# Performance work log

Hardware: AMD Instinct MI355X
Metric: run time of the kernel (lower is better)

The kernel has to match this reference:

```python
import jax, jax.numpy as jnp
import numpy as np
from jax import lax

B, MID, OUT, H, W = 16, 128, 512, 112, 112
EPS = 1e-5


def _conv(x, w, stride=1, pad=0, dil=1, groups=1):
    return lax.conv_general_dilated(
        x, w, window_strides=(stride, stride),
        padding=[(pad, pad), (pad, pad)], rhs_dilation=(dil, dil),
        feature_group_count=groups,
        dimension_numbers=('NCHW', 'OIHW', 'NCHW'))


def setup_inputs() -> dict:
    key = jax.random.key(0)
    ks = jax.random.split(key, 12)
    s = 0.05
    return {
        'x': jax.random.normal(ks[0], (B, 2 * MID, H, W), jnp.float32),
        # kernel_gen: Linear(mid, mid*9, bias=False) weight [mid*9, mid]
        'W_kg': jax.random.normal(ks[1], (MID * 9, MID), jnp.float32) * s,
        # global stream: depthwise 3x3 dil=2, then 1x1 conv, BN
        'gdw_w': jax.random.normal(ks[2], (MID, 1, 3, 3), jnp.float32) * s,
        'gdw_b': jax.random.normal(ks[3], (MID,), jnp.float32) * s,
        'gpw_w': jax.random.normal(ks[4], (MID, MID, 1, 1), jnp.float32) * s,
        'gpw_b': jax.random.normal(ks[5], (MID,), jnp.float32) * s,
        'bn1_g': jnp.ones((MID,), jnp.float32),
        'bn1_b': jnp.zeros((MID,), jnp.float32),
        'bn1_m': jax.random.normal(ks[6], (MID,), jnp.float32) * s,
        'bn1_v': jax.random.uniform(ks[7], (MID,), jnp.float32, 0.5, 1.5),
        # downsample: Conv2d(2*mid, out, 3, stride=2, pad=1), BN
        'ds_w': jax.random.normal(ks[8], (OUT, 2 * MID, 3, 3), jnp.float32) * s,
        'ds_b': jax.random.normal(ks[9], (OUT,), jnp.float32) * s,
        'bn2_g': jnp.ones((OUT,), jnp.float32),
        'bn2_b': jnp.zeros((OUT,), jnp.float32),
        'bn2_m': jax.random.normal(ks[10], (OUT,), jnp.float32) * s,
        'bn2_v': jax.random.uniform(ks[11], (OUT,), jnp.float32, 0.5, 1.5),
    }


def _bn(x, g, b, m, v):  # eval-mode BatchNorm2d
    inv = g / jnp.sqrt(v + EPS)
    return x * inv[None, :, None, None] + (b - m * inv)[None, :, None, None]


def reference(x, W_kg, gdw_w, gdw_b, gpw_w, gpw_b,
              bn1_g, bn1_b, bn1_m, bn1_v,
              ds_w, ds_b, bn2_g, bn2_b, bn2_m, bn2_v):
    local_in, global_in = jnp.split(x, 2, axis=1)  # [B,MID,H,W] each
    b, c, h, w = local_in.shape

    # local branch: pool -> linear+relu kernel-gen -> per-sample depthwise 3x3
    pooled = jnp.mean(local_in, axis=(2, 3))                  # [b,c]
    kernels = jax.nn.relu(pooled @ W_kg.T)                    # [b, c*9]
    kernels = kernels.reshape(b * c, 1, 3, 3)
    local_out = _conv(local_in.reshape(1, b * c, h, w), kernels,
                      pad=1, groups=b * c).reshape(b, c, h, w)

    # global branch: depthwise dil-2 conv -> 1x1 conv -> BN -> ReLU
    g = _conv(global_in, gdw_w, pad=2, dil=2, groups=c) + gdw_b[None, :, None, None]
    g = _conv(g, gpw_w) + gpw_b[None, :, None, None]
    g = jax.nn.relu(_bn(g, bn1_g, bn1_b, bn1_m, bn1_v))

    combined = jnp.concatenate([local_out, g], axis=1)        # [b,2c,h,w]
    out = _conv(combined, ds_w, stride=2, pad=1) + ds_b[None, :, None, None]
    out = jax.nn.relu(_bn(out, bn2_g, bn2_b, bn2_m, bn2_v))   # [b,OUT,h/2,w/2]
    return out
```

## Files before the change

### kernel.cpp

```cpp
#include <hip/hip_runtime.h>


#define DEVI static __device__ __forceinline__

using bf16x8 = __attribute__((ext_vector_type(8))) short;
using f32x4  = __attribute__((ext_vector_type(4))) float;
typedef unsigned short ushort_t;

constexpr int Bn = 16, MID = 128, CHN = 256, Hh = 112, Wn = 112;
constexpr int OHn = 56, OWn = 56, OCn = 512;
constexpr int HW  = Hh * Wn;
constexpr float EPSf = 1e-5f;

constexpr size_t C_I = 56 * 64;
constexpr size_t C_P = 4 * C_I;
constexpr size_t C_H = 2 * C_P;
constexpr size_t C_B = (size_t)Hh * C_H;

DEVI ushort_t f2b(float f) {
    unsigned u = __float_as_uint(f);
    return (ushort_t)((u + 0x7FFFu + ((u >> 16) & 1u)) >> 16);
}
DEVI float b2f(ushort_t s) { return __uint_as_float(((unsigned)s) << 16); }
DEVI int pack2(float a, float b) {
    return (int)f2b(a) | ((int)f2b(b) << 16);
}

DEVI void gl_lds16(const void* g, void* l) {
    __builtin_amdgcn_global_load_lds(
        (const __attribute__((address_space(1))) unsigned int*)g,
        (__attribute__((address_space(3))) unsigned int*)l, 16, 0, 0);
}

__global__ __launch_bounds__(256) void k_prep(
        const float* __restrict__ gpw_w, const float* __restrict__ gpw_b,
        const float* __restrict__ bn1g, const float* __restrict__ bn1b,
        const float* __restrict__ bn1m, const float* __restrict__ bn1v,
        const float* __restrict__ dsb,
        const float* __restrict__ bn2g, const float* __restrict__ bn2b,
        const float* __restrict__ bn2m, const float* __restrict__ bn2v,
        ushort_t* __restrict__ gpwbf,
        float* __restrict__ a1, float* __restrict__ b1,
        float* __restrict__ a2, float* __restrict__ b2,
        float* __restrict__ pooled) {
    int i = blockIdx.x * 256 + threadIdx.x;
    if (i < MID * MID) gpwbf[i] = f2b(gpw_w[i]);
    if (i < Bn * MID) pooled[i] = 0.f;
    if (i < OCn) {
        float inv = bn2g[i] / sqrtf(bn2v[i] + EPSf);
        a2[i] = inv;
        b2[i] = bn2b[i] + (dsb[i] - bn2m[i]) * inv;
    }
    if (i < MID) {
        float inv = bn1g[i] / sqrtf(bn1v[i] + EPSf);
        a1[i] = inv;
        b1[i] = bn1b[i] + (gpw_b[i] - bn1m[i]) * inv;
    }
}

__global__ __launch_bounds__(256) void k_wds(const float* __restrict__ dsw,
                                             ushort_t* __restrict__ wds2) {
    int d = blockIdx.x * 256 + threadIdx.x;
    int j = d & 63, oc = (d >> 6) & 511, kb = d >> 15;
    int khw = kb >> 2, icc = kb & 3;
    int ph = j >> 3, c = ph ^ (oc & 7);
    int ic = icc * 64 + c * 8 + (j & 7);
    wds2[d] = f2b(dsw[((size_t)oc * CHN + ic) * 9 + khw]);
}

__global__ __launch_bounds__(256) void k_kgen(const float* __restrict__ pooled,
                                              const float* __restrict__ wkg,
                                              float* __restrict__ kgen) {
    int idx = blockIdx.x * 256 + threadIdx.x;
    int b = idx / 1152, j = idx % 1152;
    int c = j & 127, tp = j >> 7;
    const float* pr = pooled + b * MID;
    const float* wr = wkg + (size_t)(c * 9 + tp) * MID;
    float s = 0.f;
#pragma unroll 8
    for (int i = 0; i < MID; i++) s += pr[i] * wr[i];
    kgen[idx] = fmaxf(s * (1.f / HW), 0.f);
}

__global__ __launch_bounds__(256) void k_xt(const float* __restrict__ x,
                                            ushort_t* __restrict__ xT,
                                            float* __restrict__ pooled) {
    __shared__ ushort_t tile[Wn * 264];
    int t = threadIdx.x;
    int bh = blockIdx.x;
    int b = bh / Hh, h = bh % Hh;
    const float* xp = x + ((size_t)b * CHN * Hh + h) * Wn;
    for (int idx = t; idx < CHN * 28; idx += 256) {
        int ch = idx / 28, q = idx % 28;
        float4 v = *(const float4*)(xp + (size_t)ch * HW + q * 4);
        int w = q * 4;
        tile[w * 264 + ch]       = f2b(v.x);
        tile[(w + 1) * 264 + ch] = f2b(v.y);
        tile[(w + 2) * 264 + ch] = f2b(v.z);
        tile[(w + 3) * 264 + ch] = f2b(v.w);
    }
    __syncthreads();
    int4* dst = (int4*)(xT + (size_t)bh * Wn * CHN);
    for (int q = t; q < Wn * CHN / 8; q += 256) {
        int w = q >> 5, c0 = (q & 31) << 3;
        dst[q] = *(const int4*)(tile + w * 264 + c0);
    }
    if (t < MID) {
        float s = 0.f;
        for (int w = 0; w < Wn; w++) s += b2f(tile[w * 264 + t]);
        atomicAdd(&pooled[b * MID + t], s);
    }
}

template <int DIL>
DEVI void dw_accum_row(const ushort_t* __restrict__ rp,
                       const float* __restrict__ wtab, int tb,
                       int c0, int wbase, float (&acc)[7][8]) {
    constexpr int NC = 7 + 2 * DIL;
    float wk[3][8];
#pragma unroll
    for (int dw = 0; dw < 3; dw++) {
        float4 lo = *(const float4*)&wtab[(tb + dw) * 128 + c0];
        float4 hi = *(const float4*)&wtab[(tb + dw) * 128 + c0 + 4];
        wk[dw][0] = lo.x; wk[dw][1] = lo.y; wk[dw][2] = lo.z; wk[dw][3] = lo.w;
        wk[dw][4] = hi.x; wk[dw][5] = hi.y; wk[dw][6] = hi.z; wk[dw][7] = hi.w;
    }
    int4 C[NC];
#pragma unroll
    for (int j = 0; j < NC; j++) {
        int w1 = wbase - DIL + j;
        int4 v = make_int4(0, 0, 0, 0);
        if ((unsigned)w1 < (unsigned)Wn)
            v = *(const int4*)(rp + (size_t)w1 * CHN);
        C[j] = v;
    }
#pragma unroll
    for (int j = 0; j < NC; j++) {
        float f[8];
        {
            unsigned u;
            u = (unsigned)C[j].x;
            f[0] = __uint_as_float(u << 16); f[1] = __uint_as_float(u & 0xffff0000u);
            u = (unsigned)C[j].y;
            f[2] = __uint_as_float(u << 16); f[3] = __uint_as_float(u & 0xffff0000u);
            u = (unsigned)C[j].z;
            f[4] = __uint_as_float(u << 16); f[5] = __uint_as_float(u & 0xffff0000u);
            u = (unsigned)C[j].w;
            f[6] = __uint_as_float(u << 16); f[7] = __uint_as_float(u & 0xffff0000u);
        }
#pragma unroll
        for (int dw = 0; dw < 3; dw++) {
            int i = j - dw * DIL;
            if (i >= 0 && i <= 6) {
#pragma unroll
                for (int k = 0; k < 8; k++) acc[i][k] += wk[dw][k] * f[k];
            }
        }
    }
}

__global__ __launch_bounds__(256, 3) void k_dwl(
        const ushort_t* __restrict__ xT, const float* __restrict__ kgen,
        ushort_t* __restrict__ comb) {
    __shared__ float wtab[1152];
    int t = threadIdx.x;
    int h = blockIdx.x, b = blockIdx.y;
    {
        const float4* src = (const float4*)(kgen + (size_t)b * 1152);
        float4* dstw = (float4*)wtab;
        dstw[t] = src[t];
        if (t < 32) dstw[256 + t] = src[256 + t];
    }
    __syncthreads();
    int cg = t & 15, wl = t >> 4, c0 = cg << 3, wbase = 7 * wl;
    const ushort_t* xb = xT + (size_t)b * HW * CHN + c0;
    float acc[7][8] = {};
#pragma unroll
    for (int dh = -1; dh <= 1; dh++) {
        int h1 = h + dh;
        if ((unsigned)h1 >= (unsigned)Hh) continue;
        dw_accum_row<1>(xb + (size_t)h1 * Wn * CHN, wtab, (dh + 1) * 3,
                        c0, wbase, acc);
    }
    int icc = c0 >> 6, cch = (c0 & 63) >> 3;
#pragma unroll
    for (int i = 0; i < 7; i++) {
        int w = wbase + i;
        int4 O;
        O.x = pack2(acc[i][0], acc[i][1]);
        O.y = pack2(acc[i][2], acc[i][3]);
        O.z = pack2(acc[i][4], acc[i][5]);
        O.w = pack2(acc[i][6], acc[i][7]);
        int w2 = w >> 1, p = w & 1, ph = cch ^ (w2 & 7);
        *(int4*)(comb + (size_t)b * C_B + (size_t)h * C_H + p * C_P
                 + icc * C_I + w2 * 64 + ph * 8) = O;
    }
}

__global__ __launch_bounds__(256, 3) void k_dwg(
        const ushort_t* __restrict__ xT,
        const float* __restrict__ gdw_w, const float* __restrict__ gdw_b,
        const ushort_t* __restrict__ gpwbf,
        const float* __restrict__ a1, const float* __restrict__ b1,
        ushort_t* __restrict__ comb) {
    __shared__ float wtab[1152];
    __shared__ ushort_t pbuf[112 * 136];
    int t = threadIdx.x;
    int h = blockIdx.x, b = blockIdx.y;
    for (int e4 = t; e4 < 288; e4 += 256) {
        float4 v = *(const float4*)(gdw_w + (size_t)e4 * 4);
        int e = e4 * 4;
        wtab[(e % 9) * 128 + e / 9]             = v.x;
        wtab[((e + 1) % 9) * 128 + (e + 1) / 9] = v.y;
        wtab[((e + 2) % 9) * 128 + (e + 2) / 9] = v.z;
        wtab[((e + 3) % 9) * 128 + (e + 3) / 9] = v.w;
    }
    __syncthreads();
    int cg = t & 15, wl = t >> 4, c0 = cg << 3, wbase = 7 * wl;
    const ushort_t* xb = xT + (size_t)b * HW * CHN + MID + c0;
    float acc[7][8];
    {
        float4 b0 = *(const float4*)(gdw_b + c0);
        float4 b4 = *(const float4*)(gdw_b + c0 + 4);
#pragma unroll
        for (int i = 0; i < 7; i++) {
            acc[i][0] = b0.x; acc[i][1] = b0.y; acc[i][2] = b0.z; acc[i][3] = b0.w;
            acc[i][4] = b4.x; acc[i][5] = b4.y; acc[i][6] = b4.z; acc[i][7] = b4.w;
        }
    }
#pragma unroll
    for (int dh = -1; dh <= 1; dh++) {
        int h1 = h + 2 * dh;
        if ((unsigned)h1 >= (unsigned)Hh) continue;
        dw_accum_row<2>(xb + (size_t)h1 * Wn * CHN, wtab, (dh + 1) * 3,
                        c0, wbase, acc);
    }
#pragma unroll
    for (int i = 0; i < 7; i++) {
        int w = wbase + i;
        int4 O;
        O.x = pack2(acc[i][0], acc[i][1]);
        O.y = pack2(acc[i][2], acc[i][3]);
        O.z = pack2(acc[i][4], acc[i][5]);
        O.w = pack2(acc[i][6], acc[i][7]);
        int ph = cg ^ (w & 15);
        *(int4*)(pbuf + (size_t)w * 128 + ph * 8) = O;
    }
    __syncthreads();
    int lane = t & 63, wave = t >> 6;
    int mrow = lane & 15, quad = lane >> 4;
    const short* gw = (const short*)gpwbf;
    f32x4 acc2[7][2] = {};
#pragma unroll
    for (int ks = 0; ks < 4; ks++) {
        bf16x8 bfr[2];
#pragma unroll
        for (int n = 0; n < 2; n++)
            bfr[n] = *(const bf16x8*)(gw + (size_t)(wave * 32 + n * 16 + mrow) * MID
                                         + ks * 32 + quad * 8);
#pragma unroll
        for (int m = 0; m < 7; m++) {
            int ph = (ks * 4 + quad) ^ mrow;
            bf16x8 af = *(const bf16x8*)(pbuf + (size_t)(m * 16 + mrow) * 128 + ph * 8);
#pragma unroll
            for (int n = 0; n < 2; n++)
                acc2[m][n] = __builtin_amdgcn_mfma_f32_16x16x32_bf16(
                    af, bfr[n], acc2[m][n], 0, 0, 0);
        }
    }
    __syncthreads();
#pragma unroll
    for (int m = 0; m < 7; m++)
#pragma unroll
        for (int n = 0; n < 2; n++) {
            int oc2 = wave * 32 + n * 16 + mrow;
            float al = a1[oc2], be = b1[oc2];
#pragma unroll
            for (int r = 0; r < 4; r++) {
                int px = m * 16 + quad * 4 + r;
                pbuf[px * 136 + oc2] = f2b(fmaxf(acc2[m][n][r] * al + be, 0.f));
            }
        }
    __syncthreads();
    for (int ws = 0; ws < 7; ws++) {
        int w = ws * 16 + wl;
        int4 v = *(const int4*)(pbuf + (size_t)w * 136 + c0);
        int w2 = w >> 1, p = w & 1;
        int gch = MID + c0;
        int icc = gch >> 6, cch = (gch & 63) >> 3, ph = cch ^ (w2 & 7);
        *(int4*)(comb + (size_t)b * C_B + (size_t)h * C_H + p * C_P
                 + icc * C_I + w2 * 64 + ph * 8) = v;
    }
}

__global__ __launch_bounds__(256) void k_ds(
        const ushort_t* __restrict__ comb, const ushort_t* __restrict__ wds2,
        const float* __restrict__ a2, const float* __restrict__ b2,
        float* __restrict__ out) {
    __shared__ ushort_t lA[128 * 64];
    __shared__ ushort_t lB[128 * 64];
    int t = threadIdx.x, lane = t & 63, wave = t >> 6;
    int g = blockIdx.x;
    int xcd = g & 7, s = g >> 3;
    int octile = s & 3, pl = s >> 2;
    int pair = xcd * 56 + pl;
    int bb = pair / 28, ohp = pair % 28;
    int oh0 = ohp * 2, oc0 = octile * 128;
    int mrow = lane & 15, quad = lane >> 4;
    int wm = wave & 1, wn = wave >> 1;
    int ak = mrow & 7;

    f32x4 acc[4][4] = {};
    for (int kt = 0; kt < 36; kt++) {
        int khw = kt >> 2, icc = kt & 3;
        int kh = khw / 3, kw = khw - kh * 3;
        int p = (kw == 1) ? 0 : 1;
        bool zh0 = (oh0 == 0) && (kh == 0);
        int ldsShift = (kw == 0) ? 128 : 0;
        __syncthreads();
        if (zh0) {
            int4 z = {0, 0, 0, 0};
            *(int4*)(lB + t * 8) = z;
            *(int4*)(lB + 2048 + t * 8) = z;
        }
        if (kw == 0 && t < 16) {
            int4 z = {0, 0, 0, 0};
            *(int4*)(lB + (t >> 3) * 4096 + (t & 7) * 8) = z;
        }
        const char* asrc = (const char*)wds2
            + ((size_t)kt * 32768 + (size_t)oc0 * 64) * 2 + lane * 16;
#pragma unroll
        for (int i = 0; i < 4; i++) {
            int j = wave * 4 + i;
            gl_lds16(asrc + j * 1024, (char*)lA + j * 1024);
        }
        for (int j = wave; j < 14; j += 4) {
            int osub = (j >= 7) ? 1 : 0, jj = j - osub * 7;
            if (zh0 && osub == 0) continue;
            int r = 2 * oh0 + 2 * osub + kh - 1;
            const char* bsrc = (const char*)comb
                + ((size_t)bb * C_B + (size_t)r * C_H + (size_t)p * C_P
                   + (size_t)icc * C_I) * 2 + jj * 1024 + lane * 16;
            gl_lds16(bsrc, (char*)lB + osub * 8192 + ldsShift + jj * 1024);
        }
        __syncthreads();
        int bk = (mrow + ((kw == 0) ? 7 : 0)) & 7;
#pragma unroll
        for (int ks = 0; ks < 2; ks++) {
            bf16x8 af[4], bf[4];
#pragma unroll
            for (int m = 0; m < 4; m++) {
                int row = wm * 64 + m * 16 + mrow;
                int ph = (ks * 4 + quad) ^ ak;
                af[m] = *(const bf16x8*)(lA + row * 64 + ph * 8);
            }
#pragma unroll
            for (int n = 0; n < 4; n++) {
                int nr = wn * 64 + n * 16 + mrow;
                int ph = (ks * 4 + quad) ^ bk;
                bf[n] = *(const bf16x8*)(lB + nr * 64 + ph * 8);
            }
#pragma unroll
            for (int m = 0; m < 4; m++)
#pragma unroll
                for (int n = 0; n < 4; n++)
                    acc[m][n] = __builtin_amdgcn_mfma_f32_16x16x32_bf16(
                        af[m], bf[n], acc[m][n], 0, 0, 0);
        }
    }
#pragma unroll
    for (int m = 0; m < 4; m++) {
#pragma unroll
        for (int r4 = 0; r4 < 4; r4++) {
            int oc = oc0 + wm * 64 + m * 16 + quad * 4 + r4;
            float al = a2[oc], be = b2[oc];
#pragma unroll
            for (int n = 0; n < 4; n++) {
                int nr = wn * 64 + n * 16 + mrow;
                int osub = nr >> 6, ow = nr & 63;
                if (ow < OWn) {
                    float v = fmaxf(acc[m][n][r4] * al + be, 0.f);
                    out[((size_t)(bb * OCn + oc) * OHn + (oh0 + osub)) * OWn + ow] = v;
                }
            }
        }
    }
}

extern "C" void kernel_launch(void* const* d_in, const int* in_sizes, int n_in,
                              void* d_out, int out_size, void* d_ws, size_t ws_size,
                              hipStream_t stream) {
    const float* x     = (const float*)d_in[0];
    const float* wkg   = (const float*)d_in[1];
    const float* gdw_w = (const float*)d_in[2];
    const float* gdw_b = (const float*)d_in[3];
    const float* gpw_w = (const float*)d_in[4];
    const float* gpw_b = (const float*)d_in[5];
    const float* bn1g  = (const float*)d_in[6];
    const float* bn1b  = (const float*)d_in[7];
    const float* bn1m  = (const float*)d_in[8];
    const float* bn1v  = (const float*)d_in[9];
    const float* dsw   = (const float*)d_in[10];
    const float* dsb   = (const float*)d_in[11];
    const float* bn2g  = (const float*)d_in[12];
    const float* bn2b  = (const float*)d_in[13];
    const float* bn2m  = (const float*)d_in[14];
    const float* bn2v  = (const float*)d_in[15];

    char* ws = (char*)d_ws;
    float*    pooled = (float*)(ws + 0);
    float*    kgen   = (float*)(ws + 8192);
    float*    a1     = (float*)(ws + 81920);
    float*    b1     = (float*)(ws + 82432);
    float*    a2     = (float*)(ws + 82944);
    float*    b2     = (float*)(ws + 84992);
    ushort_t* gpwbf  = (ushort_t*)(ws + 87040);
    ushort_t* wds2   = (ushort_t*)(ws + 119808);
    ushort_t* comb   = (ushort_t*)(ws + 2479104);
    ushort_t* xT  = (ushort_t*)d_out;
    float*    out = (float*)d_out;

    k_prep<<<64, 256, 0, stream>>>(gpw_w, gpw_b, bn1g, bn1b, bn1m, bn1v,
                                   dsb, bn2g, bn2b, bn2m, bn2v,
                                   gpwbf, a1, b1, a2, b2, pooled);
    k_wds <<<4608, 256, 0, stream>>>(dsw, wds2);
    k_xt  <<<1792, 256, 0, stream>>>(x, xT, pooled);
    k_kgen<<<72, 256, 0, stream>>>(pooled, wkg, kgen);
    k_dwg <<<dim3(Hh, Bn), 256, 0, stream>>>(xT, gdw_w, gdw_b, gpwbf,
                                             a1, b1, comb);
    k_dwl <<<dim3(Hh, Bn), 256, 0, stream>>>(xT, kgen, comb);
    k_ds  <<<1792, 256, 0, stream>>>(comb, wds2, a2, b2, out);
}
```

Before: 339.4 us.

## Split global branch into shared depthwise kernel and separate pointwise MFMA kernel

Merges the local and global depthwise convolutions into one kernel launched over twice the batch dimension, with a branch selecting kernel weights and dilation. The global pointwise 1x1 conv plus BN/ReLU moves into a new kernel that reloads the depthwise result from the comb buffer via direct global-to-LDS copies and writes it back in place. This is meant to free the depthwise stage from the large pbuf LDS footprint and MFMA epilogue, improving occupancy, but it adds an extra global round trip of the global-branch intermediate and one more launch.

```diff
diff --git a/kernel.cpp b/kernel.cpp
--- a/kernel.cpp
+++ b/kernel.cpp
@@ -159,30 +159,63 @@
     }
 }
 
-__global__ __launch_bounds__(256, 3) void k_dwl(
+__global__ __launch_bounds__(256, 3) void k_dw(
         const ushort_t* __restrict__ xT, const float* __restrict__ kgen,
+        const float* __restrict__ gdw_w, const float* __restrict__ gdw_b,
         ushort_t* __restrict__ comb) {
     __shared__ float wtab[1152];
     int t = threadIdx.x;
-    int h = blockIdx.x, b = blockIdx.y;
-    {
+    int h = blockIdx.x, by = blockIdx.y;
+    int b = by >> 1, br = by & 1;
+    if (br == 0) {
         const float4* src = (const float4*)(kgen + (size_t)b * 1152);
         float4* dstw = (float4*)wtab;
         dstw[t] = src[t];
         if (t < 32) dstw[256 + t] = src[256 + t];
+    } else {
+        for (int e4 = t; e4 < 288; e4 += 256) {
+            float4 v = *(const float4*)(gdw_w + (size_t)e4 * 4);
+            int e = e4 * 4;
+            wtab[(e % 9) * 128 + e / 9]             = v.x;
+            wtab[((e + 1) % 9) * 128 + (e + 1) / 9] = v.y;
+            wtab[((e + 2) % 9) * 128 + (e + 2) / 9] = v.z;
+            wtab[((e + 3) % 9) * 128 + (e + 3) / 9] = v.w;
+        }
     }
     __syncthreads();
     int cg = t & 15, wl = t >> 4, c0 = cg << 3, wbase = 7 * wl;
-    const ushort_t* xb = xT + (size_t)b * HW * CHN + c0;
-    float acc[7][8] = {};
-#pragma unroll
-    for (int dh = -1; dh <= 1; dh++) {
-        int h1 = h + dh;
-        if ((unsigned)h1 >= (unsigned)Hh) continue;
-        dw_accum_row<1>(xb + (size_t)h1 * Wn * CHN, wtab, (dh + 1) * 3,
-                        c0, wbase, acc);
-    }
-    int icc = c0 >> 6, cch = (c0 & 63) >> 3;
+    const ushort_t* xb = xT + (size_t)b * HW * CHN + (br ? MID : 0) + c0;
+    float acc[7][8];
+    if (br == 0) {
+#pragma unroll
+        for (int i = 0; i < 7; i++)
+#pragma unroll
+            for (int k = 0; k < 8; k++) acc[i][k] = 0.f;
+#pragma unroll
+        for (int dh = -1; dh <= 1; dh++) {
+            int h1 = h + dh;
+            if ((unsigned)h1 < (unsigned)Hh)
+                dw_accum_row<1>(xb + (size_t)h1 * Wn * CHN, wtab,
+                                (dh + 1) * 3, c0, wbase, acc);
+        }
+    } else {
+        float4 b0 = *(const float4*)(gdw_b + c0);
+        float4 b4 = *(const float4*)(gdw_b + c0 + 4);
+#pragma unroll
+        for (int i = 0; i < 7; i++) {
+            acc[i][0] = b0.x; acc[i][1] = b0.y; acc[i][2] = b0.z; acc[i][3] = b0.w;
+            acc[i][4] = b4.x; acc[i][5] = b4.y; acc[i][6] = b4.z; acc[i][7] = b4.w;
+        }
+#pragma unroll
+        for (int dh = -1; dh <= 1; dh++) {
+            int h1 = h + 2 * dh;
+            if ((unsigned)h1 < (unsigned)Hh)
+                dw_accum_row<2>(xb + (size_t)h1 * Wn * CHN, wtab,
+                                (dh + 1) * 3, c0, wbase, acc);
+        }
+    }
+    int gch = (br ? MID : 0) + c0;
+    int icc = gch >> 6, cch = (gch & 63) >> 3;
 #pragma unroll
     for (int i = 0; i < 7; i++) {
         int w = wbase + i;
@@ -197,57 +230,21 @@
     }
 }
 
-__global__ __launch_bounds__(256, 3) void k_dwg(
-        const ushort_t* __restrict__ xT,
-        const float* __restrict__ gdw_w, const float* __restrict__ gdw_b,
-        const ushort_t* __restrict__ gpwbf,
-        const float* __restrict__ a1, const float* __restrict__ b1,
-        ushort_t* __restrict__ comb) {
-    __shared__ float wtab[1152];
+__global__ __launch_bounds__(256, 3) void k_pw(
+        ushort_t* __restrict__ comb, const ushort_t* __restrict__ gpwbf,
+        const float* __restrict__ a1, const float* __restrict__ b1) {
     __shared__ ushort_t pbuf[112 * 136];
-    int t = threadIdx.x;
+    int t = threadIdx.x, lane = t & 63, wave = t >> 6;
     int h = blockIdx.x, b = blockIdx.y;
-    for (int e4 = t; e4 < 288; e4 += 256) {
-        float4 v = *(const float4*)(gdw_w + (size_t)e4 * 4);
-        int e = e4 * 4;
-        wtab[(e % 9) * 128 + e / 9]             = v.x;
-        wtab[((e + 1) % 9) * 128 + (e + 1) / 9] = v.y;
-        wtab[((e + 2) % 9) * 128 + (e + 2) / 9] = v.z;
-        wtab[((e + 3) % 9) * 128 + (e + 3) / 9] = v.w;
+    const char* base = (const char*)(comb + (size_t)b * C_B + (size_t)h * C_H);
+    for (int j = wave; j < 28; j += 4) {
+        int s = j / 7, cc = j - s * 7;
+        int p = s >> 1, ic = 2 + (s & 1);
+        const char* src = base + ((size_t)p * C_P + (size_t)ic * C_I) * 2
+                          + cc * 1024 + lane * 16;
+        gl_lds16(src, (char*)pbuf + (size_t)s * 7168 + cc * 1024);
     }
     __syncthreads();
-    int cg = t & 15, wl = t >> 4, c0 = cg << 3, wbase = 7 * wl;
-    const ushort_t* xb = xT + (size_t)b * HW * CHN + MID + c0;
-    float acc[7][8];
-    {
-        float4 b0 = *(const float4*)(gdw_b + c0);
-        float4 b4 = *(const float4*)(gdw_b + c0 + 4);
-#pragma unroll
-        for (int i = 0; i < 7; i++) {
-            acc[i][0] = b0.x; acc[i][1] = b0.y; acc[i][2] = b0.z; acc[i][3] = b0.w;
-            acc[i][4] = b4.x; acc[i][5] = b4.y; acc[i][6] = b4.z; acc[i][7] = b4.w;
-        }
-    }
-#pragma unroll
-    for (int dh = -1; dh <= 1; dh++) {
-        int h1 = h + 2 * dh;
-        if ((unsigned)h1 >= (unsigned)Hh) continue;
-        dw_accum_row<2>(xb + (size_t)h1 * Wn * CHN, wtab, (dh + 1) * 3,
-                        c0, wbase, acc);
-    }
-#pragma unroll
-    for (int i = 0; i < 7; i++) {
-        int w = wbase + i;
-        int4 O;
-        O.x = pack2(acc[i][0], acc[i][1]);
-        O.y = pack2(acc[i][2], acc[i][3]);
-        O.z = pack2(acc[i][4], acc[i][5]);
-        O.w = pack2(acc[i][6], acc[i][7]);
-        int ph = cg ^ (w & 15);
-        *(int4*)(pbuf + (size_t)w * 128 + ph * 8) = O;
-    }
-    __syncthreads();
-    int lane = t & 63, wave = t >> 6;
     int mrow = lane & 15, quad = lane >> 4;
     const short* gw = (const short*)gpwbf;
     f32x4 acc2[7][2] = {};
@@ -258,10 +255,16 @@
         for (int n = 0; n < 2; n++)
             bfr[n] = *(const bf16x8*)(gw + (size_t)(wave * 32 + n * 16 + mrow) * MID
                                          + ks * 32 + quad * 8);
+        int kq = ks * 4 + quad;
 #pragma unroll
         for (int m = 0; m < 7; m++) {
-            int ph = (ks * 4 + quad) ^ mrow;
-            bf16x8 af = *(const bf16x8*)(pbuf + (size_t)(m * 16 + mrow) * 128 + ph * 8);
+            int row = m * 16 + mrow;
+            int p = (row >= 56) ? 1 : 0;
+            int w2 = row - 56 * p;
+            int slab = p * 2 + (kq >> 3);
+            int ph = (kq & 7) ^ (w2 & 7);
+            bf16x8 af = *(const bf16x8*)(pbuf + (size_t)slab * 3584
+                                         + w2 * 64 + ph * 8);
 #pragma unroll
             for (int n = 0; n < 2; n++)
                 acc2[m][n] = __builtin_amdgcn_mfma_f32_16x16x32_bf16(
@@ -282,13 +285,15 @@
             }
         }
     __syncthreads();
+    int cg = t & 15, wl = t >> 4, c0 = cg << 3;
     for (int ws = 0; ws < 7; ws++) {
-        int w = ws * 16 + wl;
-        int4 v = *(const int4*)(pbuf + (size_t)w * 136 + c0);
-        int w2 = w >> 1, p = w & 1;
+        int row = ws * 16 + wl;
+        int p = (row >= 56) ? 1 : 0;
+        int w2 = row - 56 * p;
+        int4 v = *(const int4*)(pbuf + (size_t)row * 136 + c0);
         int gch = MID + c0;
         int icc = gch >> 6, cch = (gch & 63) >> 3, ph = cch ^ (w2 & 7);
-        *(int4*)(comb + (size_t)b * C_B + (size_t)h * C_H + p * C_P
+        *(int4*)(comb + (size_t)b * C_B + (size_t)h * C_H + (size_t)p * C_P
                  + icc * C_I + w2 * 64 + ph * 8) = v;
     }
 }
@@ -426,8 +431,7 @@
     k_wds <<<4608, 256, 0, stream>>>(dsw, wds2);
     k_xt  <<<1792, 256, 0, stream>>>(x, xT, pooled);
     k_kgen<<<72, 256, 0, stream>>>(pooled, wkg, kgen);
-    k_dwg <<<dim3(Hh, Bn), 256, 0, stream>>>(xT, gdw_w, gdw_b, gpwbf,
-                                             a1, b1, comb);
-    k_dwl <<<dim3(Hh, Bn), 256, 0, stream>>>(xT, kgen, comb);
+    k_dw  <<<dim3(Hh, Bn * 2), 256, 0, stream>>>(xT, kgen, gdw_w, gdw_b, comb);
+    k_pw  <<<dim3(Hh, Bn), 256, 0, stream>>>(comb, gpwbf, a1, b1);
     k_ds  <<<1792, 256, 0, stream>>>(comb, wds2, a2, b2, out);
 }
```

Measured after the change: 344.4 us. About the same (+1.5%).
